# Kernel optimization log

Hardware: AMD Instinct MI355X
Metric: run time of the kernel (lower is better)

The kernel has to match this reference:

```python
import jax, jax.numpy as jnp
import numpy as np

CLASSES = (16, 16)
CH_IN = 128
CH_LAT = 128
B, H, W = 1, 192, 256


def setup_inputs() -> dict:
    key = jax.random.key(0)
    ks = jax.random.split(key, 20)

    def w(k, shape, fan_in):
        return (jax.random.normal(k, shape, jnp.float32) / np.float32(np.sqrt(fan_in)))

    c0, c1 = CLASSES
    inp = {
        "x_in": jax.random.normal(ks[0], (B, CH_IN, H, W), jnp.float32),
        # 1x1 convs: weight [out, in], bias [out]
        "w_c11": w(ks[1], (CH_LAT, CH_IN), CH_IN), "b_c11": 0.01 * jax.random.normal(ks[2], (CH_LAT,), jnp.float32),
        "w_c12": w(ks[3], (CH_LAT, CH_LAT), CH_LAT), "b_c12": 0.01 * jax.random.normal(ks[4], (CH_LAT,), jnp.float32),
        "w_c13": w(ks[5], (c0 + 1, CH_LAT), CH_LAT), "b_c13": 0.01 * jax.random.normal(ks[6], (c0 + 1,), jnp.float32),
        # CondMul: weight [n_classes, in, out], bias [n_classes, out]
        "w_c21": w(ks[7], (c0, CH_IN, 32), CH_IN), "b_c21": 0.01 * jax.random.normal(ks[8], (c0, 32), jnp.float32),
        "w_c22": w(ks[9], (c0, 32, 32), 32), "b_c22": 0.01 * jax.random.normal(ks[10], (c0, 32), jnp.float32),
        "w_c23": w(ks[11], (c0, 32, c1), 32), "b_c23": 0.01 * jax.random.normal(ks[12], (c0, c1), jnp.float32),
        "w_r11": w(ks[13], (c0 * c1, CH_IN, 32), CH_IN), "b_r11": 0.01 * jax.random.normal(ks[14], (c0 * c1, 32), jnp.float32),
        "w_r12": w(ks[15], (c0 * c1, 32, 16), 32), "b_r12": 0.01 * jax.random.normal(ks[16], (c0 * c1, 16), jnp.float32),
        "w_r13": w(ks[17], (c0 * c1, 16, 1), 16), "b_r13": 0.01 * jax.random.normal(ks[18], (c0 * c1, 1), jnp.float32),
    }
    return inp


def _conv1x1(x, w, b):
    # x: [B,C,H,W], w: [O,C] -> [B,O,H,W]
    return jnp.einsum('bchw,oc->bohw', x, w) + b[None, :, None, None]


def _cond_mul(x, inds, w, b):
    # x: [N,in], inds: [N] int32, w: [C,in,out], b: [C,out] -> [N,out]
    return jnp.einsum('ni,nio->no', x, w[inds]) + b[inds]


def reference(x_in, w_c11, b_c11, w_c12, b_c12, w_c13, b_c13,
              w_c21, b_c21, w_c22, b_c22, w_c23, b_c23,
              w_r11, b_r11, w_r12, b_r12, w_r13, b_r13):
    lrelu = jax.nn.leaky_relu  # negative_slope=0.01, matches F.leaky_relu default
    c0, c1 = CLASSES
    total = c0 * c1

    x1 = lrelu(_conv1x1(x_in, w_c11, b_c11))
    x1 = lrelu(_conv1x1(x1, w_c12, b_c12))
    x1 = _conv1x1(x1, w_c13, b_c13)  # [B, c0+1, H, W]
    mask = lrelu(x1[:, -1:, :, :])

    # coarse routing: argmax over class logits, flattened in (B,H,W) order as in torch
    inds1 = jnp.argmax(x1[:, :c0], axis=1).reshape(-1).astype(jnp.int32)

    # tokens flattened via transpose(1,3): (B,W,H) order, faithful to original
    tok = jnp.transpose(x_in, (0, 3, 2, 1)).reshape(-1, x_in.shape[1])  # [N, CH_IN]

    x2 = lrelu(_cond_mul(tok, inds1, w_c21, b_c21))
    x2 = lrelu(_cond_mul(x2, inds1, w_c22, b_c22))
    x2 = _cond_mul(x2, inds1, w_c23, b_c23)  # [N, c1]

    inds2 = jnp.argmax(x2, axis=1).astype(jnp.int32)
    inds12 = inds1 * c0 + inds2  # original multiplies by classes[0]

    x3 = lrelu(_cond_mul(tok, inds12, w_r11, b_r11))
    x3 = lrelu(_cond_mul(x3, inds12, w_r12, b_r12))
    r = _cond_mul(x3, inds12, w_r13, b_r13).reshape(-1)  # [N]

    x_real = (inds12.astype(jnp.float32) + r) * (1.0 / float(total))
    x_real = x_real.reshape(x_in.shape[0], 1, x_in.shape[2], x_in.shape[3])
    return x_real, mask
```

## Files before the change

kernel.cpp:

```cpp
#include <hip/hip_runtime.h>

#define NPIX 49152
#define H_ 192
#define W_ 256
#define TPB 64

__global__ __launch_bounds__(256) void wtrans2_k(const float* __restrict__ Wa,
    float* __restrict__ WTa, const float* __restrict__ Wb,
    float* __restrict__ WTb, int* __restrict__ S) {
  const int b = blockIdx.x;
  const float* __restrict__ W = (b < 16) ? Wa : Wb;
  float* __restrict__ WT = (b < 16) ? WTa : WTb;
  const int bb = b & 15;
  __shared__ float tile[32][33];
  const int bx = bb & 3, by = bb >> 2;
  const int c = threadIdx.x & 31, r0 = threadIdx.x >> 5;
#pragma unroll
  for (int j = 0; j < 4; ++j) {
    const int r = r0 + j * 8;
    tile[r][c] = W[(by * 32 + r) * 128 + bx * 32 + c];
  }
  __syncthreads();
#pragma unroll
  for (int j = 0; j < 4; ++j) {
    const int r = r0 + j * 8;
    WT[(bx * 32 + r) * 128 + by * 32 + c] = tile[c][r];
  }
  if (b == 0) {
    const int t = threadIdx.x;
    if (t < 32) S[t] = 0;
    S[1088 + t] = 0;
    S[1344 + t] = 0;
  }
}

__global__ __launch_bounds__(512) void convfused_k(const float* __restrict__ X,
    const float* __restrict__ WT1, const float* __restrict__ Bv1,
    const float* __restrict__ WT2, const float* __restrict__ Bv2,
    const float* __restrict__ W3, const float* __restrict__ Bv3,
    unsigned char* __restrict__ inds1, float* __restrict__ mask_out,
    int* __restrict__ cnt1, float* __restrict__ xt) {
  __shared__ float xs2[128][64];
  __shared__ float w3s[128 * 20];
  __shared__ int lh[16];
  const int t = threadIdx.x;
  const int px = t & 63;
  const int p0 = blockIdx.x * 64;
  int ob = (t >> 6) * 16;
  ob = __builtin_amdgcn_readfirstlane(ob);
  if (t < 16) lh[t] = 0;

  const int pglob = p0 + px;
  float* __restrict__ xtp = xt + ((pglob & 255) * H_ + (pglob >> 8)) * 128;

  float acc[16];

  const float* __restrict__ W1u = WT1 + ob;
#pragma unroll
  for (int o = 0; o < 16; ++o) acc[o] = Bv1[ob + o];

  float xc[16], xn[16];
#pragma unroll
  for (int kk = 0; kk < 16; ++kk) xc[kk] = X[kk * NPIX + pglob];

  for (int ch = 0; ch < 8; ++ch) {
    const int k0 = ch * 16;
    if (ch < 7) {
#pragma unroll
      for (int kk = 0; kk < 16; ++kk)
        xn[kk] = X[(k0 + 16 + kk) * NPIX + pglob];
    }
    if (t < 64) {
#pragma unroll
      for (int q = 0; q < 4; ++q) {
        float4 v;
        v.x = xc[4 * q]; v.y = xc[4 * q + 1];
        v.z = xc[4 * q + 2]; v.w = xc[4 * q + 3];
        *(float4*)(xtp + k0 + 4 * q) = v;
      }
    }
#pragma unroll
    for (int kk = 0; kk < 16; ++kk) {
      const float xv = xc[kk];
#pragma unroll
      for (int o = 0; o < 16; ++o)
        acc[o] = fmaf(xv, W1u[(k0 + kk) * 128 + o], acc[o]);
    }
    if (ch < 7) {
#pragma unroll
      for (int kk = 0; kk < 16; ++kk) xc[kk] = xn[kk];
    }
  }
#pragma unroll
  for (int o = 0; o < 16; ++o) {
    const float v = acc[o];
    xs2[ob + o][px] = v > 0.f ? v : 0.01f * v;
  }
  __syncthreads();

  const float* __restrict__ W2u = WT2 + ob;
#pragma unroll
  for (int o = 0; o < 16; ++o) acc[o] = Bv2[ob + o];
#pragma unroll 8
  for (int k = 0; k < 128; ++k) {
    const float xv = xs2[k][px];
#pragma unroll
    for (int o = 0; o < 16; ++o)
      acc[o] = fmaf(xv, W2u[k * 128 + o], acc[o]);
  }
  __syncthreads();

#pragma unroll
  for (int o = 0; o < 16; ++o) {
    const float v = acc[o];
    xs2[ob + o][px] = v > 0.f ? v : 0.01f * v;
  }
  for (int i = t; i < 17 * 128; i += 512)
    w3s[(i & 127) * 20 + (i >> 7)] = W3[i];
  __syncthreads();

  {
    const int p = t >> 3, s = t & 7;
    float s2[2];
    s2[0] = Bv3[2 * s];
    s2[1] = Bv3[2 * s + 1];
    float m = Bv3[16];
#pragma unroll 8
    for (int k = 0; k < 128; ++k) {
      const float xv = xs2[k][p];
      float2 w2 = *(const float2*)&w3s[k * 20 + 2 * s];
      s2[0] = fmaf(xv, w2.x, s2[0]);
      s2[1] = fmaf(xv, w2.y, s2[1]);
      m = fmaf(xv, w3s[k * 20 + 16], m);
    }
    float bv = s2[0];
    int bi = 2 * s;
    if (s2[1] > bv) { bv = s2[1]; bi = 2 * s + 1; }
#pragma unroll
    for (int d = 1; d < 8; d <<= 1) {
      const float ov = __shfl_xor(bv, d, 64);
      const int oi = __shfl_xor(bi, d, 64);
      if (ov > bv || (ov == bv && oi < bi)) { bv = ov; bi = oi; }
    }
    if (s == 0) {
      inds1[p0 + p] = (unsigned char)bi;
      mask_out[p0 + p] = m > 0.f ? m : 0.01f * m;
      atomicAdd(&lh[bi], 1);
    }
  }
  __syncthreads();
  if (t < 16 && lh[t] > 0) atomicAdd(&cnt1[t], lh[t]);
}

template<int NB>
__global__ __launch_bounds__(256) void scan_desc_k(const int* __restrict__ cnt,
    int* __restrict__ off, int* __restrict__ desc, int* __restrict__ ndesc) {
  const int t = threadIdx.x;
  const int lane = t & 63, wvi = t >> 6;
  __shared__ int wsumC[4], wsumD[4];
  const int c = (t < NB) ? cnt[t] : 0;
  const int nb = (c + TPB - 1) / TPB;
  int ic = c, id = nb;
  for (int d = 1; d < 64; d <<= 1) {
    const int uc = __shfl_up(ic, d, 64);
    const int ud = __shfl_up(id, d, 64);
    if (lane >= d) { ic += uc; id += ud; }
  }
  if (lane == 63) { wsumC[wvi] = ic; wsumD[wvi] = id; }
  __syncthreads();
  int bc = 0, bd = 0;
#pragma unroll
  for (int w2 = 0; w2 < 4; ++w2) {
    if (w2 < wvi) { bc += wsumC[w2]; bd += wsumD[w2]; }
  }
  ic += bc; id += bd;
  if (t < NB) {
    off[t] = ic - c;
    const int db = id - nb;
    for (int j = 0; j < nb; ++j) desc[db + j] = (t << 12) | j;
  }
  if (t == NB - 1) *ndesc = id;
}

template<typename T>
__global__ __launch_bounds__(256) void scatter_k(const T* __restrict__ bins,
    const int* __restrict__ off, int* __restrict__ cursor,
    int* __restrict__ ord, int nbins) {
  __shared__ int lhist[256], lbase[256], lcur[256];
  const int t = threadIdx.x;
  const int n = blockIdx.x * 256 + t;
  if (t < nbins) { lhist[t] = 0; lcur[t] = 0; }
  __syncthreads();
  const int b = (int)bins[n];
  atomicAdd(&lhist[b], 1);
  __syncthreads();
  if (t < nbins && lhist[t] > 0) lbase[t] = atomicAdd(&cursor[t], lhist[t]);
  __syncthreads();
  const int r = atomicAdd(&lcur[b], 1);
  ord[off[b] + lbase[b] + r] = n;
}

__global__ __launch_bounds__(256) void chain1_k(const float* __restrict__ xt,
    const int* __restrict__ ord1, const int* __restrict__ off1,
    const int* __restrict__ cnt1, const int* __restrict__ desc1,
    const int* __restrict__ nd1,
    const float* __restrict__ wc21, const float* __restrict__ bc21,
    const float* __restrict__ wc22, const float* __restrict__ bc22,
    const float* __restrict__ wc23, const float* __restrict__ bc23,
    int* __restrict__ e12a, int* __restrict__ cnt2) {
  if ((int)blockIdx.x >= *nd1) return;
  __shared__ float w1s[4096];
  __shared__ float w2s[1024];
  __shared__ float w3s[512];
  __shared__ float bs[80];
  __shared__ float xs_[64][132];
  __shared__ int lh[16];
  const int t = threadIdx.x;
  if (t < 16) lh[t] = 0;
  const int tg = t >> 2, sub = t & 3;
  const int l0 = (t & 63) & ~3;
  const int de = desc1[blockIdx.x];
  const int e = de >> 12, chunk = de & 0xFFF;
  const int cnt = cnt1[e];
  const int pos = chunk * TPB + tg;
  const bool valid = pos < cnt;
  const int n = valid ? ord1[off1[e] + pos] : 0;

  {
    const float4* __restrict__ Wg1 = (const float4*)(wc21 + e * 4096);
#pragma unroll
    for (int j = 0; j < 4; ++j)
      *(float4*)&w1s[t * 4 + j * 1024] = Wg1[t + j * 256];
    const float4* __restrict__ Wg2 = (const float4*)(wc22 + e * 1024);
    *(float4*)&w2s[t * 4] = Wg2[t];
    if (t < 128) {
      const float4* __restrict__ Wg3 = (const float4*)(wc23 + e * 512);
      *(float4*)&w3s[t * 4] = Wg3[t];
    }
    if (t < 32) bs[t] = bc21[e * 32 + t];
    else if (t < 64) bs[t] = bc22[e * 32 + (t - 32)];
    else if (t < 80) bs[t] = bc23[e * 16 + (t - 64)];
  }
  {
    const float4* __restrict__ src = (const float4*)(xt + n * 128 + sub * 32);
    float4 tmp[8];
#pragma unroll
    for (int j = 0; j < 8; ++j) tmp[j] = src[j];
#pragma unroll
    for (int j = 0; j < 8; ++j)
      *(float4*)(&xs_[tg][sub * 32 + 4 * j]) = tmp[j];
  }
  __syncthreads();

  const int wb1 = sub * 8;
  float a[8];
#pragma unroll
  for (int o = 0; o < 8; ++o) a[o] = bs[wb1 + o];
#pragma unroll
  for (int k = 0; k < 128; k += 4) {
    float x4[4];
    *(float4*)x4 = *(const float4*)(&xs_[tg][k]);
#pragma unroll
    for (int kk = 0; kk < 4; ++kk) {
      float w8[8];
      *(float4*)&w8[0] = *(const float4*)&w1s[(k + kk) * 32 + wb1];
      *(float4*)&w8[4] = *(const float4*)&w1s[(k + kk) * 32 + wb1 + 4];
#pragma unroll
      for (int o = 0; o < 8; ++o) a[o] = fmaf(x4[kk], w8[o], a[o]);
    }
  }
#pragma unroll
  for (int o = 0; o < 8; ++o) a[o] = a[o] > 0.f ? a[o] : 0.01f * a[o];

  float b[8];
#pragma unroll
  for (int o = 0; o < 8; ++o) b[o] = bs[32 + wb1 + o];
#pragma unroll
  for (int i = 0; i < 32; ++i) {
    const float hv = __shfl(a[i & 7], l0 + (i >> 3), 64);
    float w8[8];
    *(float4*)&w8[0] = *(const float4*)&w2s[i * 32 + wb1];
    *(float4*)&w8[4] = *(const float4*)&w2s[i * 32 + wb1 + 4];
#pragma unroll
    for (int o = 0; o < 8; ++o) b[o] = fmaf(hv, w8[o], b[o]);
  }
#pragma unroll
  for (int o = 0; o < 8; ++o) b[o] = b[o] > 0.f ? b[o] : 0.01f * b[o];

  float s[4];
#pragma unroll
  for (int j = 0; j < 4; ++j) s[j] = bs[64 + sub * 4 + j];
#pragma unroll
  for (int i = 0; i < 32; ++i) {
    const float hv = __shfl(b[i & 7], l0 + (i >> 3), 64);
    float w4[4];
    *(float4*)w4 = *(const float4*)&w3s[i * 16 + sub * 4];
#pragma unroll
    for (int j = 0; j < 4; ++j) s[j] = fmaf(hv, w4[j], s[j]);
  }

  float bv = s[0];
  int bi = sub * 4;
#pragma unroll
  for (int j = 1; j < 4; ++j) {
    if (s[j] > bv) { bv = s[j]; bi = sub * 4 + j; }
  }
#pragma unroll
  for (int d = 1; d < 4; d <<= 1) {
    const float ov = __shfl_xor(bv, d, 64);
    const int oi = __shfl_xor(bi, d, 64);
    if (ov > bv || (ov == bv && oi < bi)) { bv = ov; bi = oi; }
  }
  const int e12 = e * 16 + bi;
  if (valid && sub == 0) {
    e12a[n] = e12;
    atomicAdd(&lh[bi], 1);
  }
  __syncthreads();
  if (t < 16 && lh[t] > 0)
    atomicAdd(&cnt2[e * 16 + t], lh[t]);
}

__global__ __launch_bounds__(256) void chain2_k(const float* __restrict__ xt,
    const int* __restrict__ ord2, const int* __restrict__ off2,
    const int* __restrict__ cnt2, const int* __restrict__ desc2,
    const int* __restrict__ nd2,
    const float* __restrict__ wr11, const float* __restrict__ br11,
    const float* __restrict__ wr12, const float* __restrict__ br12,
    const float* __restrict__ wr13, const float* __restrict__ br13,
    float* __restrict__ out) {
  if ((int)blockIdx.x >= *nd2) return;
  __shared__ float w1s[4096];
  __shared__ float w2s[512];
  __shared__ float w3s[16];
  __shared__ float bs[49];
  __shared__ float xs_[64][132];
  const int t = threadIdx.x;
  const int tg = t >> 2, sub = t & 3;
  const int l0 = (t & 63) & ~3;
  const int de = desc2[blockIdx.x];
  const int e12 = de >> 12, chunk = de & 0xFFF;
  const int cnt = cnt2[e12];
  const int pos = chunk * TPB + tg;
  const bool valid = pos < cnt;
  const int n = valid ? ord2[off2[e12] + pos] : 0;

  {
    const float4* __restrict__ Wg1 = (const float4*)(wr11 + e12 * 4096);
#pragma unroll
    for (int j = 0; j < 4; ++j)
      *(float4*)&w1s[t * 4 + j * 1024] = Wg1[t + j * 256];
    if (t < 128) {
      const float4* __restrict__ Wg2 = (const float4*)(wr12 + e12 * 512);
      *(float4*)&w2s[t * 4] = Wg2[t];
    }
    if (t < 16) w3s[t] = wr13[e12 * 16 + t];
    if (t < 32) bs[t] = br11[e12 * 32 + t];
    else if (t < 48) bs[t] = br12[e12 * 16 + (t - 32)];
    else if (t == 48) bs[48] = br13[e12];
  }
  {
    const float4* __restrict__ src = (const float4*)(xt + n * 128 + sub * 32);
    float4 tmp[8];
#pragma unroll
    for (int j = 0; j < 8; ++j) tmp[j] = src[j];
#pragma unroll
    for (int j = 0; j < 8; ++j)
      *(float4*)(&xs_[tg][sub * 32 + 4 * j]) = tmp[j];
  }
  __syncthreads();

  const int wb1 = sub * 8;
  float a[8];
#pragma unroll
  for (int o = 0; o < 8; ++o) a[o] = bs[wb1 + o];
#pragma unroll
  for (int k = 0; k < 128; k += 4) {
    float x4[4];
    *(float4*)x4 = *(const float4*)(&xs_[tg][k]);
#pragma unroll
    for (int kk = 0; kk < 4; ++kk) {
      float w8[8];
      *(float4*)&w8[0] = *(const float4*)&w1s[(k + kk) * 32 + wb1];
      *(float4*)&w8[4] = *(const float4*)&w1s[(k + kk) * 32 + wb1 + 4];
#pragma unroll
      for (int o = 0; o < 8; ++o) a[o] = fmaf(x4[kk], w8[o], a[o]);
    }
  }
#pragma unroll
  for (int o = 0; o < 8; ++o) a[o] = a[o] > 0.f ? a[o] : 0.01f * a[o];

  float s[4];
#pragma unroll
  for (int j = 0; j < 4; ++j) s[j] = bs[32 + sub * 4 + j];
#pragma unroll
  for (int i = 0; i < 32; ++i) {
    const float hv = __shfl(a[i & 7], l0 + (i >> 3), 64);
    float w4[4];
    *(float4*)w4 = *(const float4*)&w2s[i * 16 + sub * 4];
#pragma unroll
    for (int j = 0; j < 4; ++j) s[j] = fmaf(hv, w4[j], s[j]);
  }
#pragma unroll
  for (int j = 0; j < 4; ++j) s[j] = s[j] > 0.f ? s[j] : 0.01f * s[j];

  float r = bs[48];
#pragma unroll
  for (int i = 0; i < 16; ++i) {
    const float hv = __shfl(s[i & 3], l0 + (i >> 2), 64);
    r = fmaf(hv, w3s[i], r);
  }

  if (valid && sub == 0) out[n] = ((float)e12 + r) * (1.0f / 256.0f);
}

extern "C" void kernel_launch(void* const* d_in, const int* in_sizes, int n_in,
                              void* d_out, int out_size, void* d_ws,
                              size_t ws_size, hipStream_t stream) {
  const float* x_in  = (const float*)d_in[0];
  const float* w_c11 = (const float*)d_in[1];
  const float* b_c11 = (const float*)d_in[2];
  const float* w_c12 = (const float*)d_in[3];
  const float* b_c12 = (const float*)d_in[4];
  const float* w_c13 = (const float*)d_in[5];
  const float* b_c13 = (const float*)d_in[6];
  const float* w_c21 = (const float*)d_in[7];
  const float* b_c21 = (const float*)d_in[8];
  const float* w_c22 = (const float*)d_in[9];
  const float* b_c22 = (const float*)d_in[10];
  const float* w_c23 = (const float*)d_in[11];
  const float* b_c23 = (const float*)d_in[12];
  const float* w_r11 = (const float*)d_in[13];
  const float* b_r11 = (const float*)d_in[14];
  const float* w_r12 = (const float*)d_in[15];
  const float* b_r12 = (const float*)d_in[16];
  const float* w_r13 = (const float*)d_in[17];
  const float* b_r13 = (const float*)d_in[18];

  float* out = (float*)d_out;

  float* R0 = (float*)d_ws;
  float* R1 = R0 + 128 * NPIX;
  float* R2 = R1 + 128 * NPIX;

  float* xt = R0;
  unsigned char* inds1 = (unsigned char*)R2;
  float* wT1 = R2 + 12288;
  float* wT2 = wT1 + 16384;
  int* S = (int*)R2 + 45056;

  int* cnt1  = S;
  int* cur1  = S + 16;
  int* off1  = S + 32;
  int* nd1   = S + 48;
  int* desc1 = S + 64;
  int* cnt2  = S + 1088;
  int* cur2  = S + 1344;
  int* off2  = S + 1600;
  int* nd2   = S + 1856;
  int* desc2 = S + 1872;

  int* ib   = (int*)R1;
  int* ord1 = ib;
  int* ord2 = ib + NPIX;
  int* e12a = ib + 2 * NPIX;

  wtrans2_k<<<32, 256, 0, stream>>>(w_c11, wT1, w_c12, wT2, S);
  convfused_k<<<NPIX / 64, 512, 0, stream>>>(x_in, wT1, b_c11, wT2, b_c12,
      w_c13, b_c13, inds1, out + NPIX, cnt1, xt);
  scan_desc_k<16><<<1, 256, 0, stream>>>(cnt1, off1, desc1, nd1);
  scatter_k<unsigned char><<<NPIX / 256, 256, 0, stream>>>(inds1, off1, cur1,
                                                           ord1, 16);
  chain1_k<<<NPIX / TPB + 16, 256, 0, stream>>>(xt, ord1, off1, cnt1, desc1,
      nd1, w_c21, b_c21, w_c22, b_c22, w_c23, b_c23, e12a, cnt2);
  scan_desc_k<256><<<1, 256, 0, stream>>>(cnt2, off2, desc2, nd2);
  scatter_k<int><<<NPIX / 256, 256, 0, stream>>>(e12a, off2, cur2, ord2, 256);
  chain2_k<<<NPIX / TPB + 256, 256, 0, stream>>>(xt, ord2, off2, cnt2, desc2,
      nd2, w_r11, b_r11, w_r12, b_r12, w_r13, b_r13, out);
}
```

Baseline: 123.1 us.

## Stage input tile in LDS once and cooperatively write transposed token copy

Each of the 8 waves now loads a 16-channel slice of the 64-pixel input tile into shared memory once, replacing the loop where every wave redundantly read all 128 channels from global memory. The first 1x1 conv then reads activations from LDS. The transposed token buffer xt is written by all 512 threads reading from LDS, instead of only the first wave. The LDS row is padded to 65 to avoid bank conflicts on the transposed reads, at the cost of extra barriers and slightly more LDS.

After: 123.0 us. About the same (-0.1%).

```diff
diff --git a/kernel.cpp b/kernel.cpp
--- a/kernel.cpp
+++ b/kernel.cpp
@@ -40,7 +40,7 @@
     const float* __restrict__ W3, const float* __restrict__ Bv3,
     unsigned char* __restrict__ inds1, float* __restrict__ mask_out,
     int* __restrict__ cnt1, float* __restrict__ xt) {
-  __shared__ float xs2[128][64];
+  __shared__ float xs2[128][65];
   __shared__ float w3s[128 * 20];
   __shared__ int lh[16];
   const int t = threadIdx.x;
@@ -50,47 +50,44 @@
   ob = __builtin_amdgcn_readfirstlane(ob);
   if (t < 16) lh[t] = 0;
 
-  const int pglob = p0 + px;
-  float* __restrict__ xtp = xt + ((pglob & 255) * H_ + (pglob >> 8)) * 128;
+  {
+    float xr[16];
+#pragma unroll
+    for (int kk = 0; kk < 16; ++kk)
+      xr[kk] = X[(ob + kk) * NPIX + p0 + px];
+#pragma unroll
+    for (int kk = 0; kk < 16; ++kk)
+      xs2[ob + kk][px] = xr[kk];
+  }
+  __syncthreads();
 
   float acc[16];
 
   const float* __restrict__ W1u = WT1 + ob;
 #pragma unroll
   for (int o = 0; o < 16; ++o) acc[o] = Bv1[ob + o];
-
-  float xc[16], xn[16];
-#pragma unroll
-  for (int kk = 0; kk < 16; ++kk) xc[kk] = X[kk * NPIX + pglob];
-
-  for (int ch = 0; ch < 8; ++ch) {
-    const int k0 = ch * 16;
-    if (ch < 7) {
-#pragma unroll
-      for (int kk = 0; kk < 16; ++kk)
-        xn[kk] = X[(k0 + 16 + kk) * NPIX + pglob];
-    }
-    if (t < 64) {
-#pragma unroll
-      for (int q = 0; q < 4; ++q) {
-        float4 v;
-        v.x = xc[4 * q]; v.y = xc[4 * q + 1];
-        v.z = xc[4 * q + 2]; v.w = xc[4 * q + 3];
-        *(float4*)(xtp + k0 + 4 * q) = v;
-      }
-    }
-#pragma unroll
-    for (int kk = 0; kk < 16; ++kk) {
-      const float xv = xc[kk];
-#pragma unroll
-      for (int o = 0; o < 16; ++o)
-        acc[o] = fmaf(xv, W1u[(k0 + kk) * 128 + o], acc[o]);
-    }
-    if (ch < 7) {
-#pragma unroll
-      for (int kk = 0; kk < 16; ++kk) xc[kk] = xn[kk];
-    }
-  }
+#pragma unroll 8
+  for (int k = 0; k < 128; ++k) {
+    const float xv = xs2[k][px];
+#pragma unroll
+    for (int o = 0; o < 16; ++o)
+      acc[o] = fmaf(xv, W1u[k * 128 + o], acc[o]);
+  }
+
+#pragma unroll
+  for (int i = 0; i < 4; ++i) {
+    const int idx = t * 4 + i;
+    const int tok = idx >> 5, c4 = idx & 31;
+    const int pg = p0 + tok;
+    float4 v;
+    v.x = xs2[c4 * 4 + 0][tok];
+    v.y = xs2[c4 * 4 + 1][tok];
+    v.z = xs2[c4 * 4 + 2][tok];
+    v.w = xs2[c4 * 4 + 3][tok];
+    *(float4*)(xt + ((pg & 255) * H_ + (pg >> 8)) * 128 + c4 * 4) = v;
+  }
+  __syncthreads();
+
 #pragma unroll
   for (int o = 0; o < 16; ++o) {
     const float v = acc[o];
```
